# Performance work log

Hardware: AMD Instinct MI355X
Metric: run time of the kernel (lower is better)

Reference implementation:

```python
import jax, jax.numpy as jnp
import numpy as np

T, D = 1024, 2048
H, KH, HD = 16, 4, 128
E, K, I = 8, 2, 2048
EPS = 1e-5
CAP = 30.0          # attn logit softcap and router logit softcap
BASE = 10000.0      # rope theta


def setup_inputs() -> dict:
    key = jax.random.key(0)
    ks = jax.random.split(key, 8)
    s = 0.02
    return {
        "positions": jnp.arange(T, dtype=jnp.int32),
        "hidden_states": jax.random.normal(ks[0], (T, D), jnp.float32),
        "w_qkv": jax.random.normal(ks[1], (D, (H + 2 * KH) * HD), jnp.float32) * s,
        "w_o": jax.random.normal(ks[2], (H * HD, D), jnp.float32) * s,
        "w_gate": jax.random.normal(ks[3], (D, E), jnp.float32) * s,
        "w_gate_up": jax.random.normal(ks[4], (E, D, 2 * I), jnp.float32) * s,
        "w_down": jax.random.normal(ks[5], (E, I, D), jnp.float32) * s,
        "w_pre_attn": 1.0 + 0.01 * jax.random.normal(ks[6], (D,), jnp.float32),
        "w_post_attn": jnp.ones((D,), jnp.float32),
        "w_pre_moe": 1.0 + 0.01 * jax.random.normal(ks[7], (D,), jnp.float32),
        "w_post_moe": jnp.ones((D,), jnp.float32),
    }


def rmsnorm(x, w):
    v = jnp.mean(jnp.square(x), axis=-1, keepdims=True)
    return x * jax.lax.rsqrt(v + EPS) * w


def rope_neox(pos, x):
    # x: [T, nH, HD]; full-head-dim neox-style rotation
    half = HD // 2
    inv = 1.0 / (BASE ** (jnp.arange(half, dtype=jnp.float32) * 2.0 / HD))
    f = pos.astype(jnp.float32)[:, None] * inv            # [T, half]
    cos, sin = jnp.cos(f)[:, None, :], jnp.sin(f)[:, None, :]
    x1, x2 = x[..., :half], x[..., half:]
    return jnp.concatenate([x1 * cos - x2 * sin, x2 * cos + x1 * sin], axis=-1)


def attention(pos, x, w_qkv, w_o):
    qkv = x @ w_qkv
    q, k, v = jnp.split(qkv, [H * HD, (H + KH) * HD], axis=-1)
    q = rope_neox(pos, q.reshape(T, H, HD))
    k = rope_neox(pos, k.reshape(T, KH, HD))
    v = v.reshape(T, KH, HD)
    rep = H // KH                                          # GQA repeat
    k = jnp.repeat(k, rep, axis=1)
    v = jnp.repeat(v, rep, axis=1)
    s = jnp.einsum('qhd,khd->hqk', q, k) * (HD ** -0.5)
    s = CAP * jnp.tanh(s / CAP)                            # tanh logit cap
    causal = pos[:, None] >= pos[None, :]
    s = jnp.where(causal[None], s, -1e30)
    p = jax.nn.softmax(s, axis=-1)
    o = jnp.einsum('hqk,khd->qhd', p, v).reshape(T, H * HD)
    return o @ w_o


def moe(x, w_gate, w_gate_up, w_down):
    logits = x @ w_gate
    logits = CAP * jnp.tanh(logits / CAP)                  # router softcap
    probs = jax.nn.softmax(logits, axis=-1)
    topv, topi = jax.lax.top_k(probs, K)                   # no renorm (Grok1)
    comb = jnp.zeros((T, E), probs.dtype).at[jnp.arange(T)[:, None], topi].set(topv)
    gu = jnp.einsum('td,edf->etf', x, w_gate_up)           # [E,T,2I]
    g, u = jnp.split(gu, 2, axis=-1)
    act = jax.nn.gelu(g, approximate=True) * u             # GeluAndMul(tanh)
    out_e = jnp.einsum('eti,eid->etd', act, w_down)        # [E,T,D]
    return jnp.einsum('etd,te->td', out_e, comb)


def reference(positions, hidden_states, w_qkv, w_o, w_gate, w_gate_up, w_down,
              w_pre_attn, w_post_attn, w_pre_moe, w_post_moe):
    resid = hidden_states
    h = rmsnorm(hidden_states, w_pre_attn)
    a = attention(positions, h, w_qkv, w_o)
    resid = resid + rmsnorm(a, w_post_attn)                # post_attn_norm + add
    h = rmsnorm(resid, w_pre_moe)
    m = moe(h, w_gate, w_gate_up, w_down)
    return resid + rmsnorm(m, w_post_moe)
```

## Files before the change

kernel.cpp:

```cpp
#include <hip/hip_runtime.h>

#define TT 1024
#define DD 2048
#define NH 16
#define NKV 4
#define HDIM 128
#define NE 8
#define NI 2048
#define EPSF 1e-5f
#define NP 4

typedef short bf16x8 __attribute__((ext_vector_type(8)));
typedef float f32x4 __attribute__((ext_vector_type(4)));

__device__ __forceinline__ unsigned short f2bf(float x) {
  unsigned u = __float_as_uint(x);
  u += 0x7FFFu + ((u >> 16) & 1u);
  return (unsigned short)(u >> 16);
}
__device__ __forceinline__ float bf2f(unsigned short h) {
  return __uint_as_float((unsigned)h << 16);
}
__device__ __forceinline__ void split2(float a, unsigned short& h,
                                       unsigned short& l) {
  h = f2bf(a);
  l = f2bf(a - bf2f(h));
}

__device__ __forceinline__ float wave_sum(float v) {
#pragma unroll
  for (int m = 32; m >= 1; m >>= 1) v += __shfl_xor(v, m, 64);
  return v;
}
__device__ __forceinline__ float wave_max(float v) {
#pragma unroll
  for (int m = 32; m >= 1; m >>= 1) v = fmaxf(v, __shfl_xor(v, m, 64));
  return v;
}

__device__ __forceinline__ int swz4(int r) { return (r ^ (r >> 2)) & 3; }
__device__ __forceinline__ int swz8(int r) { return (r ^ (r >> 3)) & 7; }

__device__ __forceinline__ int swzoff(int row, int k) {
  return (k & ~31) | ((((k >> 3) & 3) ^ swz4(row & 15)) << 3) | (k & 7);
}

__device__ __forceinline__ void stage_gll(const unsigned short* src, int ld,
                                          char* ldsbase, int wid, int lane) {
#pragma unroll
  for (int j = 0; j < 2; ++j) {
    int idx = (wid * 2 + j) * 64 + lane;
    int r = idx >> 2, c = idx & 3;
    const unsigned short* g = src + (long)r * ld + c * 8;
    __builtin_amdgcn_global_load_lds(
        (const __attribute__((address_space(1))) unsigned int*)g,
        (__attribute__((address_space(3))) unsigned int*)(ldsbase +
                                                         (wid * 2 + j) * 1024),
        16, 0, 0);
  }
}
__device__ __forceinline__ void ld_frag(const char* base, int wrow, int l15,
                                        int lg, bf16x8* dst) {
#pragma unroll
  for (int i = 0; i < 4; ++i) {
    int row = wrow + i * 16 + l15;
    dst[i] = *(const bf16x8*)(base + row * 64 + ((lg ^ swz4(row)) << 4));
  }
}
__device__ __forceinline__ void mm16(const bf16x8* xa, const bf16x8* xb,
                                     f32x4 (*acc)[4]) {
#pragma unroll
  for (int mi = 0; mi < 4; ++mi)
#pragma unroll
    for (int ni = 0; ni < 4; ++ni)
      acc[mi][ni] = __builtin_amdgcn_mfma_f32_16x16x32_bf16(
          xa[mi], xb[ni], acc[mi][ni], 0, 0, 0);
}

template <int MODE>
__global__ __launch_bounds__(256) void pgemm3_k(
    const unsigned short* __restrict__ Ah, const unsigned short* __restrict__ Al,
    const unsigned short* __restrict__ Bh, const unsigned short* __restrict__ Bl,
    float* __restrict__ C, int Kh, int lda, int ldb, int ldc, long czs,
    float escale, float* __restrict__ SM, float* __restrict__ SS) {
  int z = blockIdx.z;
  int m0 = blockIdx.y * 128, n0 = blockIdx.x * 128;
  int k0 = 0, kend = Kh;
  if (MODE == 0) {
    k0 = z * Kh;
    kend = k0 + Kh;
    C += (long)z * czs;
  } else if (MODE == 1) {
    if (blockIdx.x > blockIdx.y) return;
    Ah += (long)z * TT * lda;
    Al += (long)z * TT * lda;
    Bh += (long)(z >> 2) * TT * ldb;
    Bl += (long)(z >> 2) * TT * ldb;
    C += (long)z * czs;
  } else {
    int head = z >> 2, ch = z & 3;
    int limit = (blockIdx.y + 1) * 128;
    k0 = ch * 256;
    if (k0 >= limit) return;
    kend = k0 + 256 < limit ? k0 + 256 : limit;
    Ah += (long)head * TT * lda;
    Al += (long)head * TT * lda;
    Bh += (long)(head >> 2) * HDIM * ldb;
    Bl += (long)(head >> 2) * HDIM * ldb;
    C += (long)ch * czs + head * HDIM;
  }

  __shared__ __align__(16) char lds[32768];
  int tid = threadIdx.x, lane = tid & 63, wid = tid >> 6;
  int wm = (wid >> 1) * 64, wn = (wid & 1) * 64;
  int l15 = lane & 15, lg = lane >> 4;

  f32x4 acc[4][4];
#pragma unroll
  for (int i = 0; i < 4; ++i)
#pragma unroll
    for (int j = 0; j < 4; ++j) acc[i][j] = {0.f, 0.f, 0.f, 0.f};

  for (int kt = k0; kt < kend; kt += 32) {
    __syncthreads();
    stage_gll(Ah + (long)m0 * lda + kt, lda, lds, wid, lane);
    stage_gll(Al + (long)m0 * lda + kt, lda, lds + 8192, wid, lane);
    stage_gll(Bh + (long)n0 * ldb + kt, ldb, lds + 16384, wid, lane);
    stage_gll(Bl + (long)n0 * ldb + kt, ldb, lds + 24576, wid, lane);
    __syncthreads();
    bf16x8 fah[4], fal[4], fbh[4], fbl[4];
    ld_frag(lds, wm, l15, lg, fah);
    ld_frag(lds + 16384, wn, l15, lg, fbh);
    mm16(fah, fbh, acc);
    ld_frag(lds + 24576, wn, l15, lg, fbl);
    mm16(fah, fbl, acc);
    ld_frag(lds + 8192, wm, l15, lg, fal);
    mm16(fal, fbh, acc);
  }

  if (MODE == 1) {
    int bx = blockIdx.x;
    bool diag = (bx == blockIdx.y);
    float vcap[4][4][4];
#pragma unroll
    for (int mi = 0; mi < 4; ++mi)
#pragma unroll
      for (int ni = 0; ni < 4; ++ni)
#pragma unroll
        for (int rr = 0; rr < 4; ++rr) {
          float v = acc[mi][ni][rr] * escale;
          vcap[mi][ni][rr] = 30.f * tanhf(v * (1.f / 30.f));
        }
#pragma unroll
    for (int mi = 0; mi < 4; ++mi)
#pragma unroll
      for (int ni = 0; ni < 4; ++ni)
#pragma unroll
        for (int rr = 0; rr < 4; ++rr) {
          int ml = m0 + wm + mi * 16 + lg * 4 + rr;
          int col = n0 + wn + ni * 16 + l15;
          C[(long)ml * ldc + col] = vcap[mi][ni][rr];
        }
    __syncthreads();
    float* wmx = (float*)lds;
    float* wsm = (float*)(lds + 1024);
    int ch = wid & 1;
#pragma unroll
    for (int mi = 0; mi < 4; ++mi)
#pragma unroll
      for (int rr = 0; rr < 4; ++rr) {
        int wr = wm + mi * 16 + lg * 4 + rr;
        int rowg = m0 + wr;
        float mx = -1e30f;
#pragma unroll
        for (int ni = 0; ni < 4; ++ni) {
          int colg = n0 + wn + ni * 16 + l15;
          if (!diag || colg <= rowg) mx = fmaxf(mx, vcap[mi][ni][rr]);
        }
#pragma unroll
        for (int mk = 1; mk <= 8; mk <<= 1)
          mx = fmaxf(mx, __shfl_xor(mx, mk, 64));
        if (l15 == 0) wmx[ch * 128 + wr] = mx;
      }
    __syncthreads();
#pragma unroll
    for (int mi = 0; mi < 4; ++mi)
#pragma unroll
      for (int rr = 0; rr < 4; ++rr) {
        int wr = wm + mi * 16 + lg * 4 + rr;
        int rowg = m0 + wr;
        float m2 = fmaxf(wmx[wr], wmx[128 + wr]);
        float s = 0.f;
#pragma unroll
        for (int ni = 0; ni < 4; ++ni) {
          int colg = n0 + wn + ni * 16 + l15;
          if (!diag || colg <= rowg) s += expf(vcap[mi][ni][rr] - m2);
        }
#pragma unroll
        for (int mk = 1; mk <= 8; mk <<= 1) s += __shfl_xor(s, mk, 64);
        if (l15 == 0) wsm[ch * 128 + wr] = s;
      }
    __syncthreads();
    if (tid < 128) {
      float m2 = fmaxf(wmx[tid], wmx[128 + tid]);
      float s = wsm[tid] + wsm[128 + tid];
      long so = ((long)z * 8 + bx) * TT + m0 + tid;
      SM[so] = m2;
      SS[so] = s;
    }
    return;
  }

#pragma unroll
  for (int mi = 0; mi < 4; ++mi)
#pragma unroll
    for (int ni = 0; ni < 4; ++ni)
#pragma unroll
      for (int rr = 0; rr < 4; ++rr) {
        int ml = m0 + wm + mi * 16 + lg * 4 + rr;
        int col = n0 + wn + ni * 16 + l15;
        C[(long)ml * ldc + col] = acc[mi][ni][rr];
      }
}

template <int AMODE, int EP>
__global__ __launch_bounds__(256) void gemm_k(
    const unsigned short* __restrict__ A, const float* __restrict__ Bf,
    unsigned short* __restrict__ Cb, int N, int K, int lda, int ldb, int ldc,
    long bzs, long pzs, const int* __restrict__ cnt,
    const int* __restrict__ basep, const int* __restrict__ tok,
    const int* __restrict__ slotp, const float* __restrict__ wtp,
    unsigned short* __restrict__ slots_out) {
  int z = blockIdx.z;
  int e = z >> 1, kp = z & 1;
  Bf += (long)e * bzs;
  int Me = cnt[e], be = basep[e];
  int m0 = blockIdx.y * 128, n0 = blockIdx.x * 128;
  if (m0 >= Me) return;
  int Kc = K >> 1, kbeg = kp * Kc, klim = kbeg + Kc;

  __shared__ __align__(16) char lds[32768];
  const int BOFF = 16384;
  int tid = threadIdx.x, lane = tid & 63, wid = tid >> 6;
  int wm = (wid >> 1) * 64, wn = (wid & 1) * 64;
  int l15 = lane & 15, lg = lane >> 4;

  f32x4 acc[4][4];
#pragma unroll
  for (int i = 0; i < 4; ++i)
#pragma unroll
    for (int j = 0; j < 4; ++j) acc[i][j] = {0.f, 0.f, 0.f, 0.f};

  for (int kt = kbeg; kt < klim; kt += 64) {
    __syncthreads();
#pragma unroll
    for (int i = 0; i < 4; ++i) {
      int idx = tid + i * 256;
      int r = idx >> 3, c = idx & 7;
      int gm = m0 + r;
      bf16x8 v = {0, 0, 0, 0, 0, 0, 0, 0};
      bool ok = gm < Me;
      long arow;
      if (AMODE == 1)
        arow = ok ? (long)tok[e * TT + gm] : 0;
      else
        arow = (long)be + gm;
      if (ok) v = *(const bf16x8*)(A + arow * (long)lda + kt + c * 8);
      *(bf16x8*)(lds + r * 128 + ((c ^ swz8(r)) << 4)) = v;
    }
#pragma unroll
    for (int i = 0; i < 4; ++i) {
      int gidx = tid + i * 256;
      int n = gidx & 127, kc = gidx >> 7;
      const float* src = Bf + (long)(kt + kc * 8) * ldb + n0 + n;
      bf16x8 v;
#pragma unroll
      for (int u = 0; u < 8; ++u)
        ((unsigned short*)&v)[u] = f2bf(src[(long)u * ldb]);
      *(bf16x8*)(lds + BOFF + n * 128 + ((kc ^ swz8(n)) << 4)) = v;
    }
    __syncthreads();
#pragma unroll
    for (int s = 0; s < 2; ++s) {
      bf16x8 af[4], bfr[4];
      int slotk = s * 4 + lg;
#pragma unroll
      for (int mi = 0; mi < 4; ++mi) {
        int row = wm + mi * 16 + l15;
        af[mi] =
            *(const bf16x8*)(lds + row * 128 + ((slotk ^ swz8(row)) << 4));
      }
#pragma unroll
      for (int ni = 0; ni < 4; ++ni) {
        int row = wn + ni * 16 + l15;
        bfr[ni] = *(const bf16x8*)(lds + BOFF + row * 128 +
                                   ((slotk ^ swz8(row)) << 4));
      }
      mm16(af, bfr, acc);
    }
  }
#pragma unroll
  for (int mi = 0; mi < 4; ++mi)
#pragma unroll
    for (int ni = 0; ni < 4; ++ni)
#pragma unroll
      for (int rr = 0; rr < 4; ++rr) {
        int ml = m0 + wm + mi * 16 + lg * 4 + rr;
        int col = n0 + wn + ni * 16 + l15;
        float val = acc[mi][ni][rr];
        if (ml < Me) {
          if (EP == 0) {
            Cb[(long)kp * pzs + (long)(be + ml) * ldc + col] = f2bf(val);
          } else {
            int t = tok[e * TT + ml];
            int s = slotp[e * TT + ml];
            float w = wtp[e * TT + ml];
            slots_out[(long)kp * pzs + ((long)s * TT + t) * DD + col] =
                f2bf(val * w);
          }
        }
      }
}

__global__ __launch_bounds__(256) void tsplit_k(const float* __restrict__ W,
                                                unsigned short* __restrict__ Th,
                                                unsigned short* __restrict__ Tl,
                                                int K, int N) {
  __shared__ float lds[64 * 65];
  int n0 = blockIdx.x * 64, k0 = blockIdx.y * 64;
  int tid = threadIdx.x;
#pragma unroll
  for (int i = 0; i < 4; ++i) {
    int idx = tid + i * 256;
    int kr = idx >> 4, cg = idx & 15;
    float4 v = *(const float4*)(W + (long)(k0 + kr) * N + n0 + cg * 4);
    float* p = &lds[kr * 65 + cg * 4];
    p[0] = v.x; p[1] = v.y; p[2] = v.z; p[3] = v.w;
  }
  __syncthreads();
#pragma unroll
  for (int i = 0; i < 2; ++i) {
    int idx = tid + i * 256;
    int n = idx >> 3, kc = idx & 7;
    bf16x8 h8, l8;
#pragma unroll
    for (int u = 0; u < 8; ++u) {
      unsigned short hh, ll;
      split2(lds[(kc * 8 + u) * 65 + n], hh, ll);
      ((unsigned short*)&h8)[u] = hh;
      ((unsigned short*)&l8)[u] = ll;
    }
    int row = n0 + n;
    long o = (long)row * K + swzoff(row, k0 + kc * 8);
    *(bf16x8*)(Th + o) = h8;
    *(bf16x8*)(Tl + o) = l8;
  }
}

__global__ __launch_bounds__(256) void rms_pre_k(const float* __restrict__ x,
                                                 const float* __restrict__ w,
                                                 unsigned short* __restrict__ oh,
                                                 unsigned short* __restrict__ ol) {
  __shared__ float red[4];
  int t = blockIdx.x, tid = threadIdx.x;
  const float* xr = x + (long)t * DD;
  float xv[8];
  float ss = 0.f;
#pragma unroll
  for (int i = 0; i < 8; ++i) {
    float v = xr[tid + i * 256];
    xv[i] = v;
    ss += v * v;
  }
  ss = wave_sum(ss);
  if ((tid & 63) == 0) red[tid >> 6] = ss;
  __syncthreads();
  float r = rsqrtf((red[0] + red[1] + red[2] + red[3]) * (1.f / DD) + EPSF);
#pragma unroll
  for (int i = 0; i < 8; ++i) {
    int d = tid + i * 256;
    int ds = swzoff(t, d);
    split2(xv[i] * r * w[d], oh[(long)t * DD + ds], ol[(long)t * DD + ds]);
  }
}

__global__ __launch_bounds__(256) void rope_qk_k(
    const int* __restrict__ pos, const float* __restrict__ qp,
    unsigned short* __restrict__ qh, unsigned short* __restrict__ ql,
    unsigned short* __restrict__ kh, unsigned short* __restrict__ kl) {
  __shared__ float cs[64], sn[64];
  int t = blockIdx.x, tid = threadIdx.x;
  float pf = (float)pos[t];
  if (tid < 64) {
    float inv = exp2f(-(float)tid * 0.20762050593046015f);
    float f = pf * inv;
    cs[tid] = cosf(f);
    sn[tid] = sinf(f);
  }
  __syncthreads();
  const float* row = qp + (long)t * 3072;
  const long PS = (long)TT * 3072;
#pragma unroll
  for (int i = 0; i < 4; ++i) {
    int idx = tid + i * 256;
    int h = idx >> 6, j = idx & 63;
    float x1 = 0.f, x2 = 0.f;
#pragma unroll
    for (int p = 0; p < NP; ++p) {
      x1 += row[p * PS + h * HDIM + j];
      x2 += row[p * PS + h * HDIM + 64 + j];
    }
    float c = cs[j], s = sn[j];
    long base = ((long)h * TT + t) * HDIM;
    split2(x1 * c - x2 * s, qh[base + swzoff(t, j)], ql[base + swzoff(t, j)]);
    split2(x2 * c + x1 * s, qh[base + swzoff(t, 64 + j)],
           ql[base + swzoff(t, 64 + j)]);
  }
  {
    int k2 = tid >> 6, j = tid & 63;
    float x1 = 0.f, x2 = 0.f;
#pragma unroll
    for (int p = 0; p < NP; ++p) {
      x1 += row[p * PS + 2048 + k2 * HDIM + j];
      x2 += row[p * PS + 2048 + k2 * HDIM + 64 + j];
    }
    float c = cs[j], s = sn[j];
    long base = ((long)k2 * TT + t) * HDIM;
    split2(x1 * c - x2 * s, kh[base + swzoff(t, j)], kl[base + swzoff(t, j)]);
    split2(x2 * c + x1 * s, kh[base + swzoff(t, 64 + j)],
           kl[base + swzoff(t, 64 + j)]);
  }
}

__global__ __launch_bounds__(256) void vtrans_k(const float* __restrict__ qp,
                                                unsigned short* __restrict__ Vh,
                                                unsigned short* __restrict__ Vl) {
  __shared__ float lds[64 * 129];
  int tb = blockIdx.x, kv = blockIdx.y;
  int t0 = tb * 128;
  int tid = threadIdx.x;
  const long PS = (long)TT * 3072;
#pragma unroll
  for (int dh = 0; dh < 2; ++dh) {
    if (dh) __syncthreads();
#pragma unroll
    for (int i = 0; i < 8; ++i) {
      int fidx = tid + i * 256;
      int t = fidx >> 4, dq = fidx & 15;
      long gi = (long)(t0 + t) * 3072 + 2560 + kv * HDIM + dh * 64 + dq * 4;
      float4 a = *(const float4*)(qp + gi);
#pragma unroll
      for (int p = 1; p < NP; ++p) {
        float4 b = *(const float4*)(qp + p * PS + gi);
        a.x += b.x; a.y += b.y; a.z += b.z; a.w += b.w;
      }
      lds[(dq * 4 + 0) * 129 + t] = a.x;
      lds[(dq * 4 + 1) * 129 + t] = a.y;
      lds[(dq * 4 + 2) * 129 + t] = a.z;
      lds[(dq * 4 + 3) * 129 + t] = a.w;
    }
    __syncthreads();
#pragma unroll
    for (int i = 0; i < 4; ++i) {
      int cidx = tid + i * 256;
      int d = cidx >> 4, tc = cidx & 15;
      bf16x8 h8, l8;
#pragma unroll
      for (int u = 0; u < 8; ++u) {
        unsigned short hh, ll;
        split2(lds[d * 129 + tc * 8 + u], hh, ll);
        ((unsigned short*)&h8)[u] = hh;
        ((unsigned short*)&l8)[u] = ll;
      }
      int rowd = dh * 64 + d;
      long o = ((long)kv * HDIM + rowd) * TT + swzoff(rowd, t0 + tc * 8);
      *(bf16x8*)(Vh + o) = h8;
      *(bf16x8*)(Vl + o) = l8;
    }
  }
}

__global__ __launch_bounds__(256) void softmax_k(const float* __restrict__ S,
                                                 const float* __restrict__ SM,
                                                 const float* __restrict__ SS,
                                                 unsigned short* __restrict__ Ph,
                                                 unsigned short* __restrict__ Pl) {
  int i = blockIdx.x, h = blockIdx.y, tid = threadIdx.x;
  int len = i + 1;
  int nt = (i >> 7) + 1;
  int wlimit = nt << 7;
  float m = -1e30f;
  for (int t = 0; t < nt; ++t)
    m = fmaxf(m, SM[((long)h * 8 + t) * TT + i]);
  float den = 0.f;
  for (int t = 0; t < nt; ++t) {
    long so = ((long)h * 8 + t) * TT + i;
    den += SS[so] * expf(SM[so] - m);
  }
  float inv = 1.f / den;
  const float* srow = S + ((long)h * TT + i) * TT;
  unsigned short* ph = Ph + ((long)h * TT + i) * TT;
  unsigned short* pl = Pl + ((long)h * TT + i) * TT;
  for (int j = tid; j < wlimit; j += 256) {
    float p = (j < len) ? expf(srow[j] - m) * inv : 0.f;
    unsigned short hh, ll;
    split2(p, hh, ll);
    int js = swzoff(i, j);
    ph[js] = hh;
    pl[js] = ll;
  }
}

__global__ __launch_bounds__(256) void obreduce_k(const float* __restrict__ obp,
                                                  unsigned short* __restrict__ oh,
                                                  unsigned short* __restrict__ ol) {
  int m = blockIdx.x, tid = threadIdx.x;
  int nv = ((m >> 7) >> 1) + 1;
#pragma unroll
  for (int i = 0; i < 8; ++i) {
    int d = tid + i * 256;
    float s = 0.f;
    for (int c = 0; c < nv; ++c) s += obp[(long)c * TT * DD + (long)m * DD + d];
    int ds = swzoff(m, d);
    split2(s, oh[(long)m * DD + ds], ol[(long)m * DD + ds]);
  }
}

__global__ __launch_bounds__(256) void post_attn_k(
    const float* __restrict__ ap, const float* __restrict__ hidden,
    const float* __restrict__ w_post, const float* __restrict__ w_pre2,
    float* __restrict__ resid1, float* __restrict__ h2f,
    unsigned short* __restrict__ h2b) {
  __shared__ float red[4];
  int t = blockIdx.x, tid = threadIdx.x;
  const long PS = (long)TT * DD;
  float av[8];
  float ss = 0.f;
#pragma unroll
  for (int i = 0; i < 8; ++i) {
    long o = (long)t * DD + tid + i * 256;
    float v = 0.f;
#pragma unroll
    for (int p = 0; p < NP; ++p) v += ap[p * PS + o];
    av[i] = v;
    ss += v * v;
  }
  ss = wave_sum(ss);
  if ((tid & 63) == 0) red[tid >> 6] = ss;
  __syncthreads();
  float r1 = rsqrtf((red[0] + red[1] + red[2] + red[3]) * (1.f / DD) + EPSF);
  __syncthreads();
  float rv[8];
  float ss2 = 0.f;
#pragma unroll
  for (int i = 0; i < 8; ++i) {
    int d = tid + i * 256;
    float v = hidden[(long)t * DD + d] + av[i] * r1 * w_post[d];
    rv[i] = v;
    resid1[(long)t * DD + d] = v;
    ss2 += v * v;
  }
  ss2 = wave_sum(ss2);
  if ((tid & 63) == 0) red[tid >> 6] = ss2;
  __syncthreads();
  float r2 = rsqrtf((red[0] + red[1] + red[2] + red[3]) * (1.f / DD) + EPSF);
#pragma unroll
  for (int i = 0; i < 8; ++i) {
    int d = tid + i * 256;
    float hv = rv[i] * r2 * w_pre2[d];
    h2f[(long)t * DD + d] = hv;
    h2b[(long)t * DD + d] = f2bf(hv);
  }
}

__global__ __launch_bounds__(256) void gate_k(const float* __restrict__ h2f,
                                              const float* __restrict__ wg,
                                              int* cnt, int* tok, int* slotp,
                                              float* wtp) {
  __shared__ float red[4][8];
  int t = blockIdx.x, tid = threadIdx.x;
  float a[8] = {0, 0, 0, 0, 0, 0, 0, 0};
  const float* x = h2f + (long)t * DD;
  for (int d = tid; d < DD; d += 256) {
    float xv = x[d];
    const float* wr = wg + d * 8;
#pragma unroll
    for (int e = 0; e < 8; ++e) a[e] += xv * wr[e];
  }
#pragma unroll
  for (int e = 0; e < 8; ++e) a[e] = wave_sum(a[e]);
  if ((tid & 63) == 0) {
#pragma unroll
    for (int e = 0; e < 8; ++e) red[tid >> 6][e] = a[e];
  }
  __syncthreads();
  if (tid == 0) {
    float l[8], p[8];
    float m = -1e30f;
    for (int e = 0; e < 8; ++e) {
      float v = red[0][e] + red[1][e] + red[2][e] + red[3][e];
      v = 30.f * tanhf(v * (1.f / 30.f));
      l[e] = v;
      m = fmaxf(m, v);
    }
    float s = 0.f;
    for (int e = 0; e < 8; ++e) { p[e] = expf(l[e] - m); s += p[e]; }
    for (int e = 0; e < 8; ++e) p[e] /= s;
    int i1 = 0;
    for (int e = 1; e < 8; ++e) if (p[e] > p[i1]) i1 = e;
    int i2 = (i1 == 0) ? 1 : 0;
    for (int e = 0; e < 8; ++e) if (e != i1 && p[e] > p[i2]) i2 = e;
    int q1 = atomicAdd(&cnt[i1], 1);
    tok[i1 * TT + q1] = t; slotp[i1 * TT + q1] = 0; wtp[i1 * TT + q1] = p[i1];
    int q2 = atomicAdd(&cnt[i2], 1);
    tok[i2 * TT + q2] = t; slotp[i2 * TT + q2] = 1; wtp[i2 * TT + q2] = p[i2];
  }
}

__global__ void scan_k(const int* __restrict__ cnt, int* __restrict__ basep) {
  if (threadIdx.x == 0) {
    int s = 0;
    for (int e = 0; e < NE; ++e) { basep[e] = s; s += cnt[e]; }
    basep[NE] = s;
  }
}

__global__ __launch_bounds__(256) void act_k(const unsigned short* __restrict__ gu,
                                             unsigned short* __restrict__ actb) {
  long a = blockIdx.x;
  const long PS = (long)2 * TT * 2 * NI;
  const unsigned short* g0 = gu + a * (2 * NI);
  const unsigned short* g1 = g0 + PS;
  for (int i = threadIdx.x; i < NI; i += 256) {
    float gg = bf2f(g0[i]) + bf2f(g1[i]);
    float uu = bf2f(g0[i + NI]) + bf2f(g1[i + NI]);
    float c = gg + 0.044715f * gg * gg * gg;
    float act = 0.5f * gg * (1.f + tanhf(0.7978845608028654f * c));
    actb[a * NI + i] = f2bf(act * uu);
  }
}

__global__ __launch_bounds__(256) void final_k(
    const float* __restrict__ resid1, const unsigned short* __restrict__ slots,
    const float* __restrict__ w2, float* __restrict__ out) {
  __shared__ float red[4];
  int t = blockIdx.x, tid = threadIdx.x;
  const long PL = (long)TT * DD;
  float mv[8];
  float ss = 0.f;
#pragma unroll
  for (int i = 0; i < 8; ++i) {
    long o = (long)t * DD + tid + i * 256;
    float v = bf2f(slots[o]) + bf2f(slots[PL + o]) + bf2f(slots[2 * PL + o]) +
              bf2f(slots[3 * PL + o]);
    mv[i] = v;
    ss += v * v;
  }
  ss = wave_sum(ss);
  if ((tid & 63) == 0) red[tid >> 6] = ss;
  __syncthreads();
  float r = rsqrtf((red[0] + red[1] + red[2] + red[3]) * (1.f / DD) + EPSF);
#pragma unroll
  for (int i = 0; i < 8; ++i) {
    int d = tid + i * 256;
    out[(long)t * DD + d] = resid1[(long)t * DD + d] + mv[i] * r * w2[d];
  }
}

__global__ void sentinel_k(float* out) { out[threadIdx.x] = 12345.0f; }

extern "C" void kernel_launch(void* const* d_in, const int* in_sizes, int n_in,
                              void* d_out, int out_size, void* d_ws,
                              size_t ws_size, hipStream_t stream) {
  const int* pos = (const int*)d_in[0];
  const float* hidden = (const float*)d_in[1];
  const float* w_qkv = (const float*)d_in[2];
  const float* w_o = (const float*)d_in[3];
  const float* w_gate = (const float*)d_in[4];
  const float* w_gu = (const float*)d_in[5];
  const float* w_down = (const float*)d_in[6];
  const float* w_pre_attn = (const float*)d_in[7];
  const float* w_post_attn = (const float*)d_in[8];
  const float* w_pre_moe = (const float*)d_in[9];
  const float* w_post_moe = (const float*)d_in[10];
  float* out = (float*)d_out;

  char* ws = (char*)d_ws;
  size_t off = 0;
  auto alloc = [&](size_t bytes) {
    char* p = ws + off;
    off += (bytes + 255) & ~(size_t)255;
    return p;
  };
  typedef unsigned short u16;
  u16* h1h = (u16*)alloc((size_t)TT * DD * 2);
  u16* h1l = (u16*)alloc((size_t)TT * DD * 2);
  u16* wqkvTh = (u16*)alloc((size_t)3072 * DD * 2);
  u16* wqkvTl = (u16*)alloc((size_t)3072 * DD * 2);
  float* qkvp = (float*)alloc((size_t)NP * TT * 3072 * 4);
  u16* qh_ = (u16*)alloc((size_t)NH * TT * HDIM * 2);
  u16* ql_ = (u16*)alloc((size_t)NH * TT * HDIM * 2);
  u16* kh_ = (u16*)alloc((size_t)NKV * TT * HDIM * 2);
  u16* kl_ = (u16*)alloc((size_t)NKV * TT * HDIM * 2);
  u16* vth = (u16*)alloc((size_t)NKV * HDIM * TT * 2);
  u16* vtl = (u16*)alloc((size_t)NKV * HDIM * TT * 2);
  float* S = (float*)alloc((size_t)NH * TT * TT * 4);
  float* SMb = (float*)alloc((size_t)NH * 8 * TT * 4);
  float* SSb = (float*)alloc((size_t)NH * 8 * TT * 4);
  u16* Ph = (u16*)alloc((size_t)NH * TT * TT * 2);
  u16* Pl = (u16*)alloc((size_t)NH * TT * TT * 2);
  float* obp = (float*)alloc((size_t)4 * TT * DD * 4);
  u16* obh = (u16*)alloc((size_t)TT * DD * 2);
  u16* obl = (u16*)alloc((size_t)TT * DD * 2);
  u16* woTh = (u16*)alloc((size_t)DD * DD * 2);
  u16* woTl = (u16*)alloc((size_t)DD * DD * 2);
  float* attnp = (float*)alloc((size_t)NP * TT * DD * 4);
  float* resid1 = (float*)alloc((size_t)TT * DD * 4);
  float* h2f = (float*)alloc((size_t)TT * DD * 4);
  u16* h2b = (u16*)alloc((size_t)TT * DD * 2);
  int* cnt = (int*)alloc(NE * 4);
  int* basep = (int*)alloc((NE + 1) * 4);
  int* tok = (int*)alloc((size_t)NE * TT * 4);
  int* slotp = (int*)alloc((size_t)NE * TT * 4);
  float* wtp = (float*)alloc((size_t)NE * TT * 4);
  u16* gu = (u16*)alloc((size_t)2 * 2 * TT * 2 * NI * 2);
  u16* actb = (u16*)alloc((size_t)2 * TT * NI * 2);
  u16* slots = (u16*)alloc((size_t)2 * 2 * TT * DD * 2);

  if (off > ws_size) {
    sentinel_k<<<1, 256, 0, stream>>>(out);
    return;
  }

  hipMemsetAsync(cnt, 0, NE * 4, stream);
  dim3 blk(256);

  rms_pre_k<<<TT, blk, 0, stream>>>(hidden, w_pre_attn, h1h, h1l);
  tsplit_k<<<dim3(3072 / 64, DD / 64), blk, 0, stream>>>(w_qkv, wqkvTh, wqkvTl,
                                                         DD, 3072);
  tsplit_k<<<dim3(DD / 64, DD / 64), blk, 0, stream>>>(w_o, woTh, woTl, DD, DD);

  pgemm3_k<0><<<dim3(3072 / 128, TT / 128, NP), blk, 0, stream>>>(
      h1h, h1l, wqkvTh, wqkvTl, qkvp, DD / NP, DD, DD, 3072, (long)TT * 3072,
      0.f, nullptr, nullptr);

  rope_qk_k<<<TT, blk, 0, stream>>>(pos, qkvp, qh_, ql_, kh_, kl_);
  vtrans_k<<<dim3(8, NKV), blk, 0, stream>>>(qkvp, vth, vtl);

  pgemm3_k<1><<<dim3(TT / 128, TT / 128, NH), blk, 0, stream>>>(
      qh_, ql_, kh_, kl_, S, HDIM, HDIM, HDIM, TT, (long)TT * TT,
      0.08838834764831845f, SMb, SSb);

  softmax_k<<<dim3(TT, NH), blk, 0, stream>>>(S, SMb, SSb, Ph, Pl);

  pgemm3_k<2><<<dim3(1, TT / 128, NH * 4), blk, 0, stream>>>(
      Ph, Pl, vth, vtl, obp, 256, TT, TT, DD, (long)TT * DD, 0.f, nullptr,
      nullptr);
  obreduce_k<<<TT, blk, 0, stream>>>(obp, obh, obl);

  pgemm3_k<0><<<dim3(DD / 128, TT / 128, NP), blk, 0, stream>>>(
      obh, obl, woTh, woTl, attnp, DD / NP, DD, DD, DD, (long)TT * DD, 0.f,
      nullptr, nullptr);

  post_attn_k<<<TT, blk, 0, stream>>>(attnp, hidden, w_post_attn, w_pre_moe,
                                      resid1, h2f, h2b);
  gate_k<<<TT, blk, 0, stream>>>(h2f, w_gate, cnt, tok, slotp, wtp);
  scan_k<<<1, 64, 0, stream>>>(cnt, basep);

  gemm_k<1, 0><<<dim3(2 * NI / 128, TT / 128, NE * 2), blk, 0, stream>>>(
      h2b, w_gu, gu, 2 * NI, DD, DD, 2 * NI, 2 * NI, (long)DD * 2 * NI,
      (long)2 * TT * 2 * NI, cnt, basep, tok, nullptr, nullptr, nullptr);

  act_k<<<2 * TT, blk, 0, stream>>>(gu, actb);

  gemm_k<2, 3><<<dim3(DD / 128, TT / 128, NE * 2), blk, 0, stream>>>(
      actb, w_down, nullptr, DD, NI, NI, DD, DD, (long)NI * DD,
      (long)2 * TT * DD, cnt, basep, tok, slotp, wtp, slots);

  final_k<<<TT, blk, 0, stream>>>(resid1, slots, w_post_moe, out);
}
```

Measured before the change: 493.9 us.

## Fuse softmax into PV GEMM, merge small kernels, use fast exp math

Removes the separate softmax kernel and the Ph/Pl bf16 probability buffers: the PV GEMM now reads raw fp32 scores, rebuilds row max and denominator from the partial stats, and splits the probabilities into bf16 hi/lo while staging into LDS, using 128-wide K chunks across 8 partitions. Several launches are merged (two weight transposes, rope plus V transpose, post-attn norm plus gate), which drops the h2f round-trip. The MoE A-tile staging switches to direct global-to-LDS loads, and tanhf/expf are replaced with __expf-based forms. The trade-offs are more partial-output traffic in the reduce step, repeated exp work in each PV block, and slightly lower accuracy from the fast math.

```diff
diff --git a/kernel.cpp b/kernel.cpp
--- a/kernel.cpp
+++ b/kernel.cpp
@@ -26,15 +26,14 @@
   h = f2bf(a);
   l = f2bf(a - bf2f(h));
 }
+__device__ __forceinline__ float tanh_cap30(float v) {
+  float e = __expf(v * (2.f / 30.f));
+  return 30.f - 60.f / (e + 1.f);
+}
 
 __device__ __forceinline__ float wave_sum(float v) {
 #pragma unroll
   for (int m = 32; m >= 1; m >>= 1) v += __shfl_xor(v, m, 64);
-  return v;
-}
-__device__ __forceinline__ float wave_max(float v) {
-#pragma unroll
-  for (int m = 32; m >= 1; m >>= 1) v = fmaxf(v, __shfl_xor(v, m, 64));
   return v;
 }
 
@@ -82,10 +81,13 @@
     const unsigned short* __restrict__ Ah, const unsigned short* __restrict__ Al,
     const unsigned short* __restrict__ Bh, const unsigned short* __restrict__ Bl,
     float* __restrict__ C, int Kh, int lda, int ldb, int ldc, long czs,
-    float escale, float* __restrict__ SM, float* __restrict__ SS) {
+    float escale, float* __restrict__ SM, float* __restrict__ SS,
+    const float* __restrict__ Sf) {
   int z = blockIdx.z;
   int m0 = blockIdx.y * 128, n0 = blockIdx.x * 128;
   int k0 = 0, kend = Kh;
+  const float* Sbase = nullptr;
+  int head = 0;
   if (MODE == 0) {
     k0 = z * Kh;
     kend = k0 + Kh;
@@ -98,23 +100,41 @@
     Bl += (long)(z >> 2) * TT * ldb;
     C += (long)z * czs;
   } else {
-    int head = z >> 2, ch = z & 3;
+    head = z >> 3;
+    int ch = z & 7;
     int limit = (blockIdx.y + 1) * 128;
-    k0 = ch * 256;
+    k0 = ch * 128;
     if (k0 >= limit) return;
-    kend = k0 + 256 < limit ? k0 + 256 : limit;
-    Ah += (long)head * TT * lda;
-    Al += (long)head * TT * lda;
+    kend = k0 + 128;
+    Sbase = Sf + (long)head * TT * TT;
     Bh += (long)(head >> 2) * HDIM * ldb;
     Bl += (long)(head >> 2) * HDIM * ldb;
     C += (long)ch * czs + head * HDIM;
   }
 
   __shared__ __align__(16) char lds[32768];
+  __shared__ float mrow[128], invrow[128];
   int tid = threadIdx.x, lane = tid & 63, wid = tid >> 6;
   int wm = (wid >> 1) * 64, wn = (wid & 1) * 64;
   int l15 = lane & 15, lg = lane >> 4;
 
+  if (MODE == 2) {
+    if (tid < 128) {
+      int q = m0 + tid;
+      int nt = blockIdx.y + 1;
+      float m = -1e30f;
+      for (int t = 0; t < nt; ++t)
+        m = fmaxf(m, SM[((long)head * 8 + t) * TT + q]);
+      float den = 0.f;
+      for (int t = 0; t < nt; ++t) {
+        long so = ((long)head * 8 + t) * TT + q;
+        den += SS[so] * __expf(SM[so] - m);
+      }
+      mrow[tid] = m;
+      invrow[tid] = 1.f / den;
+    }
+  }
+
   f32x4 acc[4][4];
 #pragma unroll
   for (int i = 0; i < 4; ++i)
@@ -123,8 +143,35 @@
 
   for (int kt = k0; kt < kend; kt += 32) {
     __syncthreads();
-    stage_gll(Ah + (long)m0 * lda + kt, lda, lds, wid, lane);
-    stage_gll(Al + (long)m0 * lda + kt, lda, lds + 8192, wid, lane);
+    if (MODE == 2) {
+#pragma unroll
+      for (int j = 0; j < 2; ++j) {
+        int idx = tid + j * 256;
+        int r = idx >> 2, c = idx & 3;
+        int q = m0 + r;
+        const float* sp = Sbase + (long)q * TT + kt + c * 8;
+        float4 s0 = *(const float4*)sp;
+        float4 s1 = *(const float4*)(sp + 4);
+        float mq = mrow[r], iq = invrow[r];
+        bf16x8 ph, pl;
+        int kg0 = kt + c * 8;
+#pragma unroll
+        for (int u = 0; u < 8; ++u) {
+          float s = (u < 4) ? ((const float*)&s0)[u] : ((const float*)&s1)[u - 4];
+          float p = (kg0 + u <= q) ? __expf(s - mq) * iq : 0.f;
+          unsigned short hh, ll;
+          split2(p, hh, ll);
+          ((unsigned short*)&ph)[u] = hh;
+          ((unsigned short*)&pl)[u] = ll;
+        }
+        int off = r * 64 + ((c ^ swz4(r)) << 4);
+        *(bf16x8*)(lds + off) = ph;
+        *(bf16x8*)(lds + 8192 + off) = pl;
+      }
+    } else {
+      stage_gll(Ah + (long)m0 * lda + kt, lda, lds, wid, lane);
+      stage_gll(Al + (long)m0 * lda + kt, lda, lds + 8192, wid, lane);
+    }
     stage_gll(Bh + (long)n0 * ldb + kt, ldb, lds + 16384, wid, lane);
     stage_gll(Bl + (long)n0 * ldb + kt, ldb, lds + 24576, wid, lane);
     __syncthreads();
@@ -147,10 +194,8 @@
 #pragma unroll
       for (int ni = 0; ni < 4; ++ni)
 #pragma unroll
-        for (int rr = 0; rr < 4; ++rr) {
-          float v = acc[mi][ni][rr] * escale;
-          vcap[mi][ni][rr] = 30.f * tanhf(v * (1.f / 30.f));
-        }
+        for (int rr = 0; rr < 4; ++rr)
+          vcap[mi][ni][rr] = tanh_cap30(acc[mi][ni][rr] * escale);
 #pragma unroll
     for (int mi = 0; mi < 4; ++mi)
 #pragma unroll
@@ -194,7 +239,7 @@
 #pragma unroll
         for (int ni = 0; ni < 4; ++ni) {
           int colg = n0 + wn + ni * 16 + l15;
-          if (!diag || colg <= rowg) s += expf(vcap[mi][ni][rr] - m2);
+          if (!diag || colg <= rowg) s += __expf(vcap[mi][ni][rr] - m2);
         }
 #pragma unroll
         for (int mk = 1; mk <= 8; mk <<= 1) s += __shfl_xor(s, mk, 64);
@@ -255,18 +300,21 @@
     __syncthreads();
 #pragma unroll
     for (int i = 0; i < 4; ++i) {
-      int idx = tid + i * 256;
+      int idx = (wid * 4 + i) * 64 + lane;
       int r = idx >> 3, c = idx & 7;
       int gm = m0 + r;
-      bf16x8 v = {0, 0, 0, 0, 0, 0, 0, 0};
-      bool ok = gm < Me;
       long arow;
       if (AMODE == 1)
-        arow = ok ? (long)tok[e * TT + gm] : 0;
+        arow = (gm < Me) ? (long)tok[e * TT + gm] : 0;
       else
         arow = (long)be + gm;
-      if (ok) v = *(const bf16x8*)(A + arow * (long)lda + kt + c * 8);
-      *(bf16x8*)(lds + r * 128 + ((c ^ swz8(r)) << 4)) = v;
+      int cs = c ^ swz8(r);
+      const unsigned short* g = A + arow * (long)lda + kt + cs * 8;
+      __builtin_amdgcn_global_load_lds(
+          (const __attribute__((address_space(1))) unsigned int*)g,
+          (__attribute__((address_space(3))) unsigned int*)(lds +
+                                                           (wid * 4 + i) * 1024),
+          16, 0, 0);
     }
 #pragma unroll
     for (int i = 0; i < 4; ++i) {
@@ -322,12 +370,22 @@
       }
 }
 
-__global__ __launch_bounds__(256) void tsplit_k(const float* __restrict__ W,
-                                                unsigned short* __restrict__ Th,
-                                                unsigned short* __restrict__ Tl,
-                                                int K, int N) {
+__global__ __launch_bounds__(256) void tsplit2_k(
+    const float* __restrict__ Wq, unsigned short* __restrict__ Thq,
+    unsigned short* __restrict__ Tlq, const float* __restrict__ Wo,
+    unsigned short* __restrict__ Tho, unsigned short* __restrict__ Tlo) {
   __shared__ float lds[64 * 65];
-  int n0 = blockIdx.x * 64, k0 = blockIdx.y * 64;
+  int b = blockIdx.x;
+  const float* W;
+  unsigned short *Th, *Tl;
+  int K = DD, N, bx, by;
+  if (b < 1536) {
+    W = Wq; Th = Thq; Tl = Tlq; N = 3072; bx = b % 48; by = b / 48;
+  } else {
+    int b2 = b - 1536;
+    W = Wo; Th = Tho; Tl = Tlo; N = DD; bx = b2 % 32; by = b2 / 32;
+  }
+  int n0 = bx * 64, k0 = by * 64;
   int tid = threadIdx.x;
 #pragma unroll
   for (int i = 0; i < 4; ++i) {
@@ -384,130 +442,99 @@
   }
 }
 
-__global__ __launch_bounds__(256) void rope_qk_k(
+__global__ __launch_bounds__(256) void ropevt_k(
     const int* __restrict__ pos, const float* __restrict__ qp,
     unsigned short* __restrict__ qh, unsigned short* __restrict__ ql,
-    unsigned short* __restrict__ kh, unsigned short* __restrict__ kl) {
-  __shared__ float cs[64], sn[64];
-  int t = blockIdx.x, tid = threadIdx.x;
-  float pf = (float)pos[t];
-  if (tid < 64) {
-    float inv = exp2f(-(float)tid * 0.20762050593046015f);
-    float f = pf * inv;
-    cs[tid] = cosf(f);
-    sn[tid] = sinf(f);
-  }
-  __syncthreads();
-  const float* row = qp + (long)t * 3072;
+    unsigned short* __restrict__ kh, unsigned short* __restrict__ kl,
+    unsigned short* __restrict__ Vh, unsigned short* __restrict__ Vl) {
+  __shared__ __align__(16) float smem[64 * 129];
+  int b = blockIdx.x, tid = threadIdx.x;
   const long PS = (long)TT * 3072;
-#pragma unroll
-  for (int i = 0; i < 4; ++i) {
-    int idx = tid + i * 256;
-    int h = idx >> 6, j = idx & 63;
-    float x1 = 0.f, x2 = 0.f;
-#pragma unroll
-    for (int p = 0; p < NP; ++p) {
-      x1 += row[p * PS + h * HDIM + j];
-      x2 += row[p * PS + h * HDIM + 64 + j];
-    }
-    float c = cs[j], s = sn[j];
-    long base = ((long)h * TT + t) * HDIM;
-    split2(x1 * c - x2 * s, qh[base + swzoff(t, j)], ql[base + swzoff(t, j)]);
-    split2(x2 * c + x1 * s, qh[base + swzoff(t, 64 + j)],
-           ql[base + swzoff(t, 64 + j)]);
-  }
-  {
-    int k2 = tid >> 6, j = tid & 63;
-    float x1 = 0.f, x2 = 0.f;
-#pragma unroll
-    for (int p = 0; p < NP; ++p) {
-      x1 += row[p * PS + 2048 + k2 * HDIM + j];
-      x2 += row[p * PS + 2048 + k2 * HDIM + 64 + j];
-    }
-    float c = cs[j], s = sn[j];
-    long base = ((long)k2 * TT + t) * HDIM;
-    split2(x1 * c - x2 * s, kh[base + swzoff(t, j)], kl[base + swzoff(t, j)]);
-    split2(x2 * c + x1 * s, kh[base + swzoff(t, 64 + j)],
-           kl[base + swzoff(t, 64 + j)]);
-  }
-}
-
-__global__ __launch_bounds__(256) void vtrans_k(const float* __restrict__ qp,
-                                                unsigned short* __restrict__ Vh,
-                                                unsigned short* __restrict__ Vl) {
-  __shared__ float lds[64 * 129];
-  int tb = blockIdx.x, kv = blockIdx.y;
-  int t0 = tb * 128;
-  int tid = threadIdx.x;
-  const long PS = (long)TT * 3072;
-#pragma unroll
-  for (int dh = 0; dh < 2; ++dh) {
-    if (dh) __syncthreads();
-#pragma unroll
-    for (int i = 0; i < 8; ++i) {
-      int fidx = tid + i * 256;
-      int t = fidx >> 4, dq = fidx & 15;
-      long gi = (long)(t0 + t) * 3072 + 2560 + kv * HDIM + dh * 64 + dq * 4;
-      float4 a = *(const float4*)(qp + gi);
-#pragma unroll
-      for (int p = 1; p < NP; ++p) {
-        float4 b = *(const float4*)(qp + p * PS + gi);
-        a.x += b.x; a.y += b.y; a.z += b.z; a.w += b.w;
-      }
-      lds[(dq * 4 + 0) * 129 + t] = a.x;
-      lds[(dq * 4 + 1) * 129 + t] = a.y;
-      lds[(dq * 4 + 2) * 129 + t] = a.z;
-      lds[(dq * 4 + 3) * 129 + t] = a.w;
+  if (b < TT) {
+    float* cs = smem;
+    float* sn = smem + 64;
+    int t = b;
+    float pf = (float)pos[t];
+    if (tid < 64) {
+      float inv = exp2f(-(float)tid * 0.20762050593046015f);
+      float f = pf * inv;
+      cs[tid] = cosf(f);
+      sn[tid] = sinf(f);
     }
     __syncthreads();
+    const float* row = qp + (long)t * 3072;
 #pragma unroll
     for (int i = 0; i < 4; ++i) {
-      int cidx = tid + i * 256;
-      int d = cidx >> 4, tc = cidx & 15;
-      bf16x8 h8, l8;
-#pragma unroll
-      for (int u = 0; u < 8; ++u) {
-        unsigned short hh, ll;
-        split2(lds[d * 129 + tc * 8 + u], hh, ll);
-        ((unsigned short*)&h8)[u] = hh;
-        ((unsigned short*)&l8)[u] = ll;
-      }
-      int rowd = dh * 64 + d;
-      long o = ((long)kv * HDIM + rowd) * TT + swzoff(rowd, t0 + tc * 8);
-      *(bf16x8*)(Vh + o) = h8;
-      *(bf16x8*)(Vl + o) = l8;
-    }
-  }
-}
-
-__global__ __launch_bounds__(256) void softmax_k(const float* __restrict__ S,
-                                                 const float* __restrict__ SM,
-                                                 const float* __restrict__ SS,
-                                                 unsigned short* __restrict__ Ph,
-                                                 unsigned short* __restrict__ Pl) {
-  int i = blockIdx.x, h = blockIdx.y, tid = threadIdx.x;
-  int len = i + 1;
-  int nt = (i >> 7) + 1;
-  int wlimit = nt << 7;
-  float m = -1e30f;
-  for (int t = 0; t < nt; ++t)
-    m = fmaxf(m, SM[((long)h * 8 + t) * TT + i]);
-  float den = 0.f;
-  for (int t = 0; t < nt; ++t) {
-    long so = ((long)h * 8 + t) * TT + i;
-    den += SS[so] * expf(SM[so] - m);
-  }
-  float inv = 1.f / den;
-  const float* srow = S + ((long)h * TT + i) * TT;
-  unsigned short* ph = Ph + ((long)h * TT + i) * TT;
-  unsigned short* pl = Pl + ((long)h * TT + i) * TT;
-  for (int j = tid; j < wlimit; j += 256) {
-    float p = (j < len) ? expf(srow[j] - m) * inv : 0.f;
-    unsigned short hh, ll;
-    split2(p, hh, ll);
-    int js = swzoff(i, j);
-    ph[js] = hh;
-    pl[js] = ll;
+      int idx = tid + i * 256;
+      int h = idx >> 6, j = idx & 63;
+      float x1 = 0.f, x2 = 0.f;
+#pragma unroll
+      for (int p = 0; p < NP; ++p) {
+        x1 += row[p * PS + h * HDIM + j];
+        x2 += row[p * PS + h * HDIM + 64 + j];
+      }
+      float c = cs[j], s = sn[j];
+      long base = ((long)h * TT + t) * HDIM;
+      split2(x1 * c - x2 * s, qh[base + swzoff(t, j)], ql[base + swzoff(t, j)]);
+      split2(x2 * c + x1 * s, qh[base + swzoff(t, 64 + j)],
+             ql[base + swzoff(t, 64 + j)]);
+    }
+    {
+      int k2 = tid >> 6, j = tid & 63;
+      float x1 = 0.f, x2 = 0.f;
+#pragma unroll
+      for (int p = 0; p < NP; ++p) {
+        x1 += row[p * PS + 2048 + k2 * HDIM + j];
+        x2 += row[p * PS + 2048 + k2 * HDIM + 64 + j];
+      }
+      float c = cs[j], s = sn[j];
+      long base = ((long)k2 * TT + t) * HDIM;
+      split2(x1 * c - x2 * s, kh[base + swzoff(t, j)], kl[base + swzoff(t, j)]);
+      split2(x2 * c + x1 * s, kh[base + swzoff(t, 64 + j)],
+             kl[base + swzoff(t, 64 + j)]);
+    }
+  } else {
+    int bb = b - TT;
+    int tb = bb & 7, kv = bb >> 3;
+    int t0 = tb * 128;
+#pragma unroll
+    for (int dh = 0; dh < 2; ++dh) {
+      if (dh) __syncthreads();
+#pragma unroll
+      for (int i = 0; i < 8; ++i) {
+        int fidx = tid + i * 256;
+        int t = fidx >> 4, dq = fidx & 15;
+        long gi = (long)(t0 + t) * 3072 + 2560 + kv * HDIM + dh * 64 + dq * 4;
+        float4 a = *(const float4*)(qp + gi);
+#pragma unroll
+        for (int p = 1; p < NP; ++p) {
+          float4 bb4 = *(const float4*)(qp + p * PS + gi);
+          a.x += bb4.x; a.y += bb4.y; a.z += bb4.z; a.w += bb4.w;
+        }
+        smem[(dq * 4 + 0) * 129 + t] = a.x;
+        smem[(dq * 4 + 1) * 129 + t] = a.y;
+        smem[(dq * 4 + 2) * 129 + t] = a.z;
+        smem[(dq * 4 + 3) * 129 + t] = a.w;
+      }
+      __syncthreads();
+#pragma unroll
+      for (int i = 0; i < 4; ++i) {
+        int cidx = tid + i * 256;
+        int d = cidx >> 4, tc = cidx & 15;
+        bf16x8 h8, l8;
+#pragma unroll
+        for (int u = 0; u < 8; ++u) {
+          unsigned short hh, ll;
+          split2(smem[d * 129 + tc * 8 + u], hh, ll);
+          ((unsigned short*)&h8)[u] = hh;
+          ((unsigned short*)&l8)[u] = ll;
+        }
+        int rowd = dh * 64 + d;
+        long o = ((long)kv * HDIM + rowd) * TT + swzoff(rowd, t0 + tc * 8);
+        *(bf16x8*)(Vh + o) = h8;
+        *(bf16x8*)(Vl + o) = l8;
+      }
+    }
   }
 }
 
@@ -515,7 +542,7 @@
                                                   unsigned short* __restrict__ oh,
                                                   unsigned short* __restrict__ ol) {
   int m = blockIdx.x, tid = threadIdx.x;
-  int nv = ((m >> 7) >> 1) + 1;
+  int nv = (m >> 7) + 1;
 #pragma unroll
   for (int i = 0; i < 8; ++i) {
     int d = tid + i * 256;
@@ -526,12 +553,14 @@
   }
 }
 
-__global__ __launch_bounds__(256) void post_attn_k(
+__global__ __launch_bounds__(256) void post_attn_gate_k(
     const float* __restrict__ ap, const float* __restrict__ hidden,
     const float* __restrict__ w_post, const float* __restrict__ w_pre2,
-    float* __restrict__ resid1, float* __restrict__ h2f,
-    unsigned short* __restrict__ h2b) {
+    const float* __restrict__ wg, float* __restrict__ resid1,
+    unsigned short* __restrict__ h2b, int* cnt, int* tok, int* slotp,
+    float* wtp) {
   __shared__ float red[4];
+  __shared__ float red8[4][8];
   int t = blockIdx.x, tid = threadIdx.x;
   const long PS = (long)TT * DD;
   float av[8];
@@ -564,41 +593,28 @@
   if ((tid & 63) == 0) red[tid >> 6] = ss2;
   __syncthreads();
   float r2 = rsqrtf((red[0] + red[1] + red[2] + red[3]) * (1.f / DD) + EPSF);
+  float a[8] = {0, 0, 0, 0, 0, 0, 0, 0};
 #pragma unroll
   for (int i = 0; i < 8; ++i) {
     int d = tid + i * 256;
     float hv = rv[i] * r2 * w_pre2[d];
-    h2f[(long)t * DD + d] = hv;
     h2b[(long)t * DD + d] = f2bf(hv);
-  }
-}
-
-__global__ __launch_bounds__(256) void gate_k(const float* __restrict__ h2f,
-                                              const float* __restrict__ wg,
-                                              int* cnt, int* tok, int* slotp,
-                                              float* wtp) {
-  __shared__ float red[4][8];
-  int t = blockIdx.x, tid = threadIdx.x;
-  float a[8] = {0, 0, 0, 0, 0, 0, 0, 0};
-  const float* x = h2f + (long)t * DD;
-  for (int d = tid; d < DD; d += 256) {
-    float xv = x[d];
     const float* wr = wg + d * 8;
 #pragma unroll
-    for (int e = 0; e < 8; ++e) a[e] += xv * wr[e];
+    for (int e = 0; e < 8; ++e) a[e] += hv * wr[e];
   }
 #pragma unroll
   for (int e = 0; e < 8; ++e) a[e] = wave_sum(a[e]);
   if ((tid & 63) == 0) {
 #pragma unroll
-    for (int e = 0; e < 8; ++e) red[tid >> 6][e] = a[e];
+    for (int e = 0; e < 8; ++e) red8[tid >> 6][e] = a[e];
   }
   __syncthreads();
   if (tid == 0) {
     float l[8], p[8];
     float m = -1e30f;
     for (int e = 0; e < 8; ++e) {
-      float v = red[0][e] + red[1][e] + red[2][e] + red[3][e];
+      float v = red8[0][e] + red8[1][e] + red8[2][e] + red8[3][e];
       v = 30.f * tanhf(v * (1.f / 30.f));
       l[e] = v;
       m = fmaxf(m, v);
@@ -634,9 +650,10 @@
   for (int i = threadIdx.x; i < NI; i += 256) {
     float gg = bf2f(g0[i]) + bf2f(g1[i]);
     float uu = bf2f(g0[i + NI]) + bf2f(g1[i + NI]);
-    float c = gg + 0.044715f * gg * gg * gg;
-    float act = 0.5f * gg * (1.f + tanhf(0.7978845608028654f * c));
-    actb[a * NI + i] = f2bf(act * uu);
+    float y = 0.7978845608028654f * (gg + 0.044715f * gg * gg * gg);
+    float ey = __expf(2.f * y);
+    float th = 1.f - 2.f / (ey + 1.f);
+    actb[a * NI + i] = f2bf(0.5f * gg * (1.f + th) * uu);
   }
 }
 
@@ -707,16 +724,13 @@
   float* S = (float*)alloc((size_t)NH * TT * TT * 4);
   float* SMb = (float*)alloc((size_t)NH * 8 * TT * 4);
   float* SSb = (float*)alloc((size_t)NH * 8 * TT * 4);
-  u16* Ph = (u16*)alloc((size_t)NH * TT * TT * 2);
-  u16* Pl = (u16*)alloc((size_t)NH * TT * TT * 2);
-  float* obp = (float*)alloc((size_t)4 * TT * DD * 4);
+  float* obp = (float*)alloc((size_t)8 * TT * DD * 4);
   u16* obh = (u16*)alloc((size_t)TT * DD * 2);
   u16* obl = (u16*)alloc((size_t)TT * DD * 2);
   u16* woTh = (u16*)alloc((size_t)DD * DD * 2);
   u16* woTl = (u16*)alloc((size_t)DD * DD * 2);
   float* attnp = (float*)alloc((size_t)NP * TT * DD * 4);
   float* resid1 = (float*)alloc((size_t)TT * DD * 4);
-  float* h2f = (float*)alloc((size_t)TT * DD * 4);
   u16* h2b = (u16*)alloc((size_t)TT * DD * 2);
   int* cnt = (int*)alloc(NE * 4);
   int* basep = (int*)alloc((NE + 1) * 4);
@@ -736,35 +750,31 @@
   dim3 blk(256);
 
   rms_pre_k<<<TT, blk, 0, stream>>>(hidden, w_pre_attn, h1h, h1l);
-  tsplit_k<<<dim3(3072 / 64, DD / 64), blk, 0, stream>>>(w_qkv, wqkvTh, wqkvTl,
-                                                         DD, 3072);
-  tsplit_k<<<dim3(DD / 64, DD / 64), blk, 0, stream>>>(w_o, woTh, woTl, DD, DD);
+  tsplit2_k<<<2560, blk, 0, stream>>>(w_qkv, wqkvTh, wqkvTl, w_o, woTh, woTl);
 
   pgemm3_k<0><<<dim3(3072 / 128, TT / 128, NP), blk, 0, stream>>>(
       h1h, h1l, wqkvTh, wqkvTl, qkvp, DD / NP, DD, DD, 3072, (long)TT * 3072,
-      0.f, nullptr, nullptr);
-
-  rope_qk_k<<<TT, blk, 0, stream>>>(pos, qkvp, qh_, ql_, kh_, kl_);
-  vtrans_k<<<dim3(8, NKV), blk, 0, stream>>>(qkvp, vth, vtl);
+      0.f, nullptr, nullptr, nullptr);
+
+  ropevt_k<<<TT + 32, blk, 0, stream>>>(pos, qkvp, qh_, ql_, kh_, kl_, vth,
+                                        vtl);
 
   pgemm3_k<1><<<dim3(TT / 128, TT / 128, NH), blk, 0, stream>>>(
       qh_, ql_, kh_, kl_, S, HDIM, HDIM, HDIM, TT, (long)TT * TT,
-      0.08838834764831845f, SMb, SSb);
-
-  softmax_k<<<dim3(TT, NH), blk, 0, stream>>>(S, SMb, SSb, Ph, Pl);
-
-  pgemm3_k<2><<<dim3(1, TT / 128, NH * 4), blk, 0, stream>>>(
-      Ph, Pl, vth, vtl, obp, 256, TT, TT, DD, (long)TT * DD, 0.f, nullptr,
-      nullptr);
+      0.08838834764831845f, SMb, SSb, nullptr);
+
+  pgemm3_k<2><<<dim3(1, TT / 128, NH * 8), blk, 0, stream>>>(
+      nullptr, nullptr, vth, vtl, obp, 128, TT, TT, DD, (long)TT * DD, 0.f,
+      SMb, SSb, S);
   obreduce_k<<<TT, blk, 0, stream>>>(obp, obh, obl);
 
   pgemm3_k<0><<<dim3(DD / 128, TT / 128, NP), blk, 0, stream>>>(
       obh, obl, woTh, woTl, attnp, DD / NP, DD, DD, DD, (long)TT * DD, 0.f,
-      nullptr, nullptr);
-
-  post_attn_k<<<TT, blk, 0, stream>>>(attnp, hidden, w_post_attn, w_pre_moe,
-                                      resid1, h2f, h2b);
-  gate_k<<<TT, blk, 0, stream>>>(h2f, w_gate, cnt, tok, slotp, wtp);
+      nullptr, nullptr, nullptr);
+
+  post_attn_gate_k<<<TT, blk, 0, stream>>>(attnp, hidden, w_post_attn,
+                                           w_pre_moe, w_gate, resid1, h2b, cnt,
+                                           tok, slotp, wtp);
   scan_k<<<1, 64, 0, stream>>>(cnt, basep);
 
   gemm_k<1, 0><<<dim3(2 * NI / 128, TT / 128, NE * 2), blk, 0, stream>>>(
```

New measurement: 455.0 us. 1.09x faster.
